# Optimization experiments

Hardware: AMD Instinct MI355X
Metric: run time of the kernel (lower is better)

## Reference

```python
import jax, jax.numpy as jnp
import numpy as np
import math

D_MODEL = 1024
N_HEADS = 16
D_K = 64
CHUNK_LEN = 64


def setup_inputs() -> dict:
    key = jax.random.key(0)
    ks = jax.random.split(key, 12)
    hd = N_HEADS * D_K
    s = 0.02
    return {
        'h': jax.random.normal(ks[0], (4, 2048, D_MODEL), jnp.float32),
        'e': jax.random.normal(ks[1], (4, 32, 2, 128, D_MODEL), jnp.float32),
        'Wq': jax.random.normal(ks[2], (D_MODEL, hd), jnp.float32) * s,
        'bq': jnp.zeros((hd,), jnp.float32),
        'Wk': jax.random.normal(ks[3], (D_MODEL, hd), jnp.float32) * s,
        'bk': jnp.zeros((hd,), jnp.float32),
        'Wv': jax.random.normal(ks[4], (D_MODEL, hd), jnp.float32) * s,
        'bv': jnp.zeros((hd,), jnp.float32),
        'Wo': jax.random.normal(ks[5], (hd, D_MODEL), jnp.float32) * s,
        'bo': jnp.zeros((D_MODEL,), jnp.float32),
        'gamma': jnp.ones((D_MODEL,), jnp.float32),
        'beta': jnp.zeros((D_MODEL,), jnp.float32),
    }


def reference(h, e, Wq, bq, Wk, bk, Wv, bv, Wo, bo, gamma, beta):
    b, chunks, neighbors, nlen, d_model = e.shape
    seq_len = h.shape[1]
    scale = 1.0 / math.sqrt(D_K)
    h_res = h
    # shift so chunk i attends to neighbors retrieved for chunk i
    hh = h[:, CHUNK_LEN - 1:]
    # layer norm
    mu = jnp.mean(hh, axis=-1, keepdims=True)
    var = jnp.mean(jnp.square(hh - mu), axis=-1, keepdims=True)
    hh = (hh - mu) / jnp.sqrt(var + 1e-5) * gamma + beta
    # pad to chunks * CHUNK_LEN
    pad = chunks * CHUNK_LEN - hh.shape[1]
    hh = jnp.pad(hh, ((0, 0), (0, pad), (0, 0)))
    hh = hh.reshape(b, chunks, CHUNK_LEN, d_model)
    q = (hh @ Wq + bq).reshape(b, chunks, CHUNK_LEN, N_HEADS, D_K)
    k = (e @ Wk + bk).reshape(b, chunks, neighbors, nlen, N_HEADS, D_K)
    v = (e @ Wv + bv).reshape(b, chunks, neighbors, nlen, N_HEADS, D_K)
    attn = jnp.einsum('bcihd,bcnjhd->bchinj', q, k) * scale  # [b,c,h,i,n,j]
    a_shape = attn.shape
    attn = jax.nn.softmax(attn.reshape(*a_shape[:-2], -1), axis=-1).reshape(a_shape)
    out = jnp.einsum('bchinj,bcnjhd->bcihd', attn, v)
    out = out.reshape(b, chunks * CHUNK_LEN, N_HEADS * D_K)
    out = out @ Wo + bo
    out = jnp.pad(out, ((0, 0), (CHUNK_LEN - 1, 0), (0, 0)))
    return out[:, :seq_len] + h_res
```

## Files before the change

### kernel.cpp

```cpp
#include <hip/hip_runtime.h>
#include <cstdint>
#include <cstddef>


typedef float f32x4 __attribute__((ext_vector_type(4)));
typedef __bf16 bf16x8 __attribute__((ext_vector_type(8)));

static __device__ __forceinline__ ushort f2bf(float f) {
  union { float f; uint32_t u; } x; x.f = f;
  uint32_t r = x.u + 0x7fffu + ((x.u >> 16) & 1u);
  return (ushort)(r >> 16);
}

static __device__ __forceinline__ bf16x8 ld_frag(const ushort* p) {
  union { uint4 u; bf16x8 v; } x;
  x.u = *(const uint4*)p;
  return x.v;
}

static __device__ __forceinline__ bf16x8 u4_frag(uint4 u) {
  union { uint4 u; bf16x8 v; } x;
  x.u = u;
  return x.v;
}

static __device__ __forceinline__ void gl2lds16(const ushort* g, ushort* l) {
  __builtin_amdgcn_global_load_lds(
      (const __attribute__((address_space(1))) void*)g,
      (__attribute__((address_space(3))) void*)l,
      16, 0, 0);
}

__global__ __launch_bounds__(256) void transpose_cast4(const float* __restrict__ Wq,
                                                       const float* __restrict__ Wk,
                                                       const float* __restrict__ Wv,
                                                       const float* __restrict__ Wo,
                                                       ushort* __restrict__ WqT,
                                                       ushort* __restrict__ WkvT,
                                                       ushort* __restrict__ WoT) {
  const float* W; ushort* WT;
  switch (blockIdx.z) {
    case 0:  W = Wq; WT = WqT; break;
    case 1:  W = Wk; WT = WkvT; break;
    case 2:  W = Wv; WT = WkvT + (size_t)1024 * 1024; break;
    default: W = Wo; WT = WoT; break;
  }
  __shared__ float tile[64][65];
  const int t = threadIdx.x;
  const int n0 = blockIdx.x * 64, k0 = blockIdx.y * 64;
#pragma unroll
  for (int i = 0; i < 4; ++i) {
    int lid = i * 256 + t;
    int r = lid >> 4, c4 = (lid & 15) * 4;
    float4 v = *(const float4*)&W[(size_t)(k0 + r) * 1024 + n0 + c4];
    tile[r][c4 + 0] = v.x; tile[r][c4 + 1] = v.y;
    tile[r][c4 + 2] = v.z; tile[r][c4 + 3] = v.w;
  }
  __syncthreads();
#pragma unroll
  for (int i = 0; i < 4; ++i) {
    int lid = i * 256 + t;
    int n = lid >> 4, k4 = (lid & 15) * 4;
    ushort4 o;
    o.x = f2bf(tile[k4 + 0][n]); o.y = f2bf(tile[k4 + 1][n]);
    o.z = f2bf(tile[k4 + 2][n]); o.w = f2bf(tile[k4 + 3][n]);
    *(ushort4*)&WT[(size_t)(n0 + n) * 1024 + k0 + k4] = o;
  }
}

__global__ __launch_bounds__(256) void cast_bf16(const float* __restrict__ x,
                                                 ushort* __restrict__ y) {
  const size_t i = ((size_t)blockIdx.x * 256 + threadIdx.x) * 8;
  float4 a = *(const float4*)&x[i];
  float4 b = *(const float4*)&x[i + 4];
  ushort o[8];
  o[0] = f2bf(a.x); o[1] = f2bf(a.y); o[2] = f2bf(a.z); o[3] = f2bf(a.w);
  o[4] = f2bf(b.x); o[5] = f2bf(b.y); o[6] = f2bf(b.z); o[7] = f2bf(b.w);
  *(uint4*)&y[i] = *(const uint4*)o;
}

__global__ __launch_bounds__(256) void ln_kernel(const float* __restrict__ h,
                                                 const float* __restrict__ gamma,
                                                 const float* __restrict__ beta,
                                                 ushort* __restrict__ hh) {
  const int bx = blockIdx.x;
  const int b = bx >> 11, s = bx & 2047;
  const int t = threadIdx.x;
  ushort* orow = hh + (size_t)(b * 2048 + s) * 1024;
  if (s >= 1985) {
    ushort4 z; z.x = 0; z.y = 0; z.z = 0; z.w = 0;
    *(ushort4*)&orow[t * 4] = z;
    return;
  }
  const float* xrow = h + (size_t)(b * 2048 + 63 + s) * 1024;
  float4 x = *(const float4*)&xrow[t * 4];
  float s1 = x.x + x.y + x.z + x.w;
  float s2 = x.x * x.x + x.y * x.y + x.z * x.z + x.w * x.w;
#pragma unroll
  for (int off = 32; off > 0; off >>= 1) {
    s1 += __shfl_xor(s1, off);
    s2 += __shfl_xor(s2, off);
  }
  __shared__ float a1[4], a2[4];
  if ((t & 63) == 0) { a1[t >> 6] = s1; a2[t >> 6] = s2; }
  __syncthreads();
  s1 = a1[0] + a1[1] + a1[2] + a1[3];
  s2 = a2[0] + a2[1] + a2[2] + a2[3];
  const float mu = s1 * (1.0f / 1024.0f);
  const float var = s2 * (1.0f / 1024.0f) - mu * mu;
  const float rstd = rsqrtf(var + 1e-5f);
  float4 g = *(const float4*)&gamma[t * 4];
  float4 be = *(const float4*)&beta[t * 4];
  ushort4 o;
  o.x = f2bf((x.x - mu) * rstd * g.x + be.x);
  o.y = f2bf((x.y - mu) * rstd * g.y + be.y);
  o.z = f2bf((x.z - mu) * rstd * g.z + be.z);
  o.w = f2bf((x.w - mu) * rstd * g.w + be.w);
  *(ushort4*)&orow[t * 4] = o;
}

template <int MODE, int NT>
__global__ __launch_bounds__(256) void gemm_bf16(const ushort* __restrict__ A,
                                                 const ushort* __restrict__ Bt,
                                                 const float* __restrict__ bias,
                                                 const float* __restrict__ bias2,
                                                 ushort* __restrict__ Cbf,
                                                 ushort* __restrict__ Vtg,
                                                 float* __restrict__ Cf,
                                                 const float* __restrict__ resid,
                                                 int mtiles, float scale,
                                                 int mrow_off) {
  if constexpr (MODE == 1) {
    if (blockIdx.x >= 512) {
      const int idx4 = (blockIdx.x - 512) * 256 + threadIdx.x;
      const int b = idx4 / 16128;
      const int rem = idx4 - b * 16128;
      const size_t o = (size_t)b * 2048 * 1024 + (size_t)rem * 4;
      *(float4*)&Cf[o] = *(const float4*)&resid[o];
      return;
    }
  }
  __shared__ __align__(16) ushort Alds[2][128 * 32];
  __shared__ __align__(16) ushort Blds[2][128 * 32];
  const int t = threadIdx.x;
  const int lane = t & 63, wave = t >> 6;
  const int quad = lane >> 4, l16 = lane & 15;

  const int L = blockIdx.x;
  const int xcd = L & 7, slot = L >> 3;
  const int nt = slot & (NT - 1);
  const int mt = xcd * (mtiles >> 3) + (slot / NT);
  const int m0 = mt * 128, n0 = nt * 128;

  const int srow = lane >> 2;
  const int scol = (lane & 3) * 8;
  const int c0 = wave * 2;
  const ushort* gA0 = A  + (size_t)(m0 + c0 * 16 + srow) * 1024 + scol;
  const ushort* gA1 = gA0 + 16 * 1024;
  const ushort* gB0 = Bt + (size_t)(n0 + c0 * 16 + srow) * 1024 + scol;
  const ushort* gB1 = gB0 + 16 * 1024;
  ushort* dA0 = &Alds[0][c0 * 512 + lane * 8];
  ushort* dA1 = dA0 + 512;
  ushort* dB0 = &Blds[0][c0 * 512 + lane * 8];
  ushort* dB1 = dB0 + 512;
  const ptrdiff_t SUB = 128 * 32;

  const int wrow = (wave >> 1) * 64, wcol = (wave & 1) * 64;
  const ushort* pA = &Alds[0][(wrow + l16) * 32 + quad * 8];
  const ushort* pB = &Blds[0][(wcol + l16) * 32 + quad * 8];

  f32x4 zero = {0.f, 0.f, 0.f, 0.f};
  f32x4 acc[4][4];
#pragma unroll
  for (int i = 0; i < 4; ++i)
#pragma unroll
    for (int j = 0; j < 4; ++j) acc[i][j] = zero;

  for (int kb = 0; kb < 16; ++kb) {
    const int ko = kb * 64;
    gl2lds16(gA0 + ko, dA0);         gl2lds16(gA1 + ko, dA1);
    gl2lds16(gA0 + ko + 32, dA0 + SUB); gl2lds16(gA1 + ko + 32, dA1 + SUB);
    gl2lds16(gB0 + ko, dB0);         gl2lds16(gB1 + ko, dB1);
    gl2lds16(gB0 + ko + 32, dB0 + SUB); gl2lds16(gB1 + ko + 32, dB1 + SUB);
    __syncthreads();
#pragma unroll
    for (int sub = 0; sub < 2; ++sub) {
      bf16x8 af[4], bfv[4];
#pragma unroll
      for (int i = 0; i < 4; ++i) af[i]  = ld_frag(pA + sub * SUB + i * 512);
#pragma unroll
      for (int j = 0; j < 4; ++j) bfv[j] = ld_frag(pB + sub * SUB + j * 512);
#pragma unroll
      for (int i = 0; i < 4; ++i)
#pragma unroll
        for (int j = 0; j < 4; ++j)
          acc[i][j] = __builtin_amdgcn_mfma_f32_16x16x32_bf16(af[i], bfv[j], acc[i][j], 0, 0, 0);
    }
    __syncthreads();
  }

#pragma unroll
  for (int mi = 0; mi < 4; ++mi)
#pragma unroll
    for (int mj = 0; mj < 4; ++mj) {
      const int cc = n0 + wcol + mj * 16 + l16;
      const int r0 = m0 + wrow + mi * 16 + quad * 4;
      if constexpr (MODE == 0) {
        const float bvb = bias[cc];
#pragma unroll
        for (int rr = 0; rr < 4; ++rr)
          Cbf[(size_t)(r0 + rr) * 1024 + cc] = f2bf((acc[mi][mj][rr] + bvb) * scale);
      } else {
        const float bvb = bias[cc];
#pragma unroll
        for (int rr = 0; rr < 4; ++rr) {
          const int r = r0 + rr;
          const int b = r >> 11, s = r & 2047;
          if (s < 1985) {
            const size_t o = (size_t)(b * 2048 + s + 63) * 1024 + cc;
            Cf[o] = acc[mi][mj][rr] + bvb + resid[o];
          }
        }
      }
    }
}

__global__ __launch_bounds__(512, 2) void gemm_kv256(const ushort* __restrict__ A,
                                                     const ushort* __restrict__ Bt,
                                                     const float* __restrict__ bk_,
                                                     const float* __restrict__ bv_,
                                                     ushort* __restrict__ Kout,
                                                     ushort* __restrict__ Vtg,
                                                     int mrow_off) {
  __shared__ __align__(16) ushort Alds[4 * 8192];
  __shared__ __align__(16) ushort Blds[4 * 8192];

  const int t = threadIdx.x;
  const int lane = t & 63, wave = t >> 6;
  const int wm = wave >> 2, wn = wave & 3;
  const int l16 = lane & 15, quad = lane >> 4;

  const int L = blockIdx.x;
  const int xcd = L & 7, slot = L >> 3;
  const int nt = slot & 7, mt = xcd * 8 + (slot >> 3);
  const int m0 = mt * 256, n0 = nt * 256;

  const int w2 = wave * 2;
  const int srow = lane >> 3;
  const int lanex = (lane & 7) ^ srow;
  const ushort* gA2 = A  + (size_t)(m0 + w2 * 8 + srow) * 1024 + lanex * 8;
  const ushort* gB2 = Bt + (size_t)(n0 + w2 * 8 + srow) * 1024 + lanex * 8;
  ushort* dA2 = Alds + w2 * 512 + lane * 8;
  ushort* dB2 = Blds + w2 * 512 + lane * 8;

  auto stage_a = [&](int ti, int hh) {
    const ushort* g = gA2 + (size_t)hh * 131072 + (size_t)ti * 64;
    ushort* d = dA2 + ((ti & 1) * 2 + hh) * 8192;
    gl2lds16(g, d);
    gl2lds16(g + 8192, d + 512);
  };
  auto stage_b = [&](int ti, int hh) {
    const ushort* g = gB2 + (size_t)hh * 131072 + (size_t)ti * 64;
    ushort* d = dB2 + ((ti & 1) * 2 + hh) * 8192;
    gl2lds16(g, d);
    gl2lds16(g + 8192, d + 512);
  };

  const int b2 = (l16 >> 2) & 1;
  const int qx = (quad ^ (l16 & 3)) << 3;
  const int kof0 = b2 << 5;
  const int kof1 = 32 - kof0;

  f32x4 zero = {0.f, 0.f, 0.f, 0.f};
  f32x4 acc[8][4];
#pragma unroll
  for (int i = 0; i < 8; ++i)
#pragma unroll
    for (int j = 0; j < 4; ++j) acc[i][j] = zero;

  stage_b(0, 0); stage_a(0, 0); stage_b(0, 1); stage_a(0, 1);
  stage_b(1, 0); stage_a(1, 0); stage_b(1, 1);
  asm volatile("s_waitcnt vmcnt(6)" ::: "memory");
  __builtin_amdgcn_s_barrier();

  bf16x8 a[4][2], b01[2][2], b23[2][2];

#pragma unroll 2
  for (int tt = 0; tt < 16; ++tt) {
    const int cur = tt & 1;
    const ushort* pa = Alds + (cur * 2 + wm) * 8192 + l16 * 64 + qx;
    const ushort* pb = Blds + (cur * 2 + (wn >> 1)) * 8192 +
                       ((wn & 1) * 64 + l16) * 64 + qx;

#pragma unroll
    for (int mi = 0; mi < 4; ++mi) {
      a[mi][0] = ld_frag(pa + mi * 1024 + kof0);
      a[mi][1] = ld_frag(pa + mi * 1024 + kof1);
    }
#pragma unroll
    for (int ni = 0; ni < 2; ++ni) {
      b01[ni][0] = ld_frag(pb + ni * 1024 + kof0);
      b01[ni][1] = ld_frag(pb + ni * 1024 + kof1);
    }
    if (tt < 15) stage_a(tt + 1, 1);
    __builtin_amdgcn_s_barrier();
    asm volatile("s_waitcnt lgkmcnt(0)" ::: "memory");
    __builtin_amdgcn_sched_barrier(0);
    __builtin_amdgcn_s_setprio(1);
#pragma unroll
    for (int mi = 0; mi < 4; ++mi)
#pragma unroll
      for (int ni = 0; ni < 2; ++ni) {
        acc[mi][ni] = __builtin_amdgcn_mfma_f32_16x16x32_bf16(a[mi][0], b01[ni][0], acc[mi][ni], 0, 0, 0);
        acc[mi][ni] = __builtin_amdgcn_mfma_f32_16x16x32_bf16(a[mi][1], b01[ni][1], acc[mi][ni], 0, 0, 0);
      }
    __builtin_amdgcn_s_setprio(0);
    __builtin_amdgcn_s_barrier();

#pragma unroll
    for (int ni = 0; ni < 2; ++ni) {
      b23[ni][0] = ld_frag(pb + (ni + 2) * 1024 + kof0);
      b23[ni][1] = ld_frag(pb + (ni + 2) * 1024 + kof1);
    }
    if (tt < 14) stage_b(tt + 2, 0);
    __builtin_amdgcn_s_barrier();
    asm volatile("s_waitcnt lgkmcnt(0)" ::: "memory");
    __builtin_amdgcn_sched_barrier(0);
    __builtin_amdgcn_s_setprio(1);
#pragma unroll
    for (int mi = 0; mi < 4; ++mi)
#pragma unroll
      for (int ni = 0; ni < 2; ++ni) {
        acc[mi][ni + 2] = __builtin_amdgcn_mfma_f32_16x16x32_bf16(a[mi][0], b23[ni][0], acc[mi][ni + 2], 0, 0, 0);
        acc[mi][ni + 2] = __builtin_amdgcn_mfma_f32_16x16x32_bf16(a[mi][1], b23[ni][1], acc[mi][ni + 2], 0, 0, 0);
      }
    __builtin_amdgcn_s_setprio(0);
    __builtin_amdgcn_s_barrier();

#pragma unroll
    for (int mi = 0; mi < 4; ++mi) {
      a[mi][0] = ld_frag(pa + (mi + 4) * 1024 + kof0);
      a[mi][1] = ld_frag(pa + (mi + 4) * 1024 + kof1);
    }
    if (tt < 14) stage_b(tt + 2, 1);
    __builtin_amdgcn_s_barrier();
    asm volatile("s_waitcnt lgkmcnt(0)" ::: "memory");
    __builtin_amdgcn_sched_barrier(0);
    __builtin_amdgcn_s_setprio(1);
#pragma unroll
    for (int mi = 0; mi < 4; ++mi)
#pragma unroll
      for (int ni = 0; ni < 2; ++ni) {
        acc[mi + 4][ni + 2] = __builtin_amdgcn_mfma_f32_16x16x32_bf16(a[mi][0], b23[ni][0], acc[mi + 4][ni + 2], 0, 0, 0);
        acc[mi + 4][ni + 2] = __builtin_amdgcn_mfma_f32_16x16x32_bf16(a[mi][1], b23[ni][1], acc[mi + 4][ni + 2], 0, 0, 0);
      }
    __builtin_amdgcn_s_setprio(0);
    __builtin_amdgcn_s_barrier();

    if (tt < 14) stage_a(tt + 2, 0);
    __builtin_amdgcn_s_barrier();
    __builtin_amdgcn_s_setprio(1);
#pragma unroll
    for (int mi = 0; mi < 4; ++mi)
#pragma unroll
      for (int ni = 0; ni < 2; ++ni) {
        acc[mi + 4][ni] = __builtin_amdgcn_mfma_f32_16x16x32_bf16(a[mi][0], b01[ni][0], acc[mi + 4][ni], 0, 0, 0);
        acc[mi + 4][ni] = __builtin_amdgcn_mfma_f32_16x16x32_bf16(a[mi][1], b01[ni][1], acc[mi + 4][ni], 0, 0, 0);
      }
    __builtin_amdgcn_s_setprio(0);
    if (tt < 15) {
      if (tt == 14) asm volatile("s_waitcnt vmcnt(0)" ::: "memory");
      else          asm volatile("s_waitcnt vmcnt(6)" ::: "memory");
      __builtin_amdgcn_s_barrier();
    }
  }

  const int rbase = m0 + wm * 128 + quad * 4;
  const int cbase = n0 + wn * 64 + l16;
  if (n0 < 1024) {
#pragma unroll
    for (int mi = 0; mi < 8; ++mi)
#pragma unroll
      for (int ni = 0; ni < 4; ++ni) {
        const int cc = cbase + ni * 16;
        const float bb = bk_[cc];
        const int r0 = rbase + mi * 16;
#pragma unroll
        for (int rr = 0; rr < 4; ++rr)
          Kout[(size_t)(r0 + rr) * 1024 + cc] = f2bf(acc[mi][ni][rr] + bb);
      }
  } else {
#pragma unroll
    for (int mi = 0; mi < 8; ++mi)
#pragma unroll
      for (int ni = 0; ni < 4; ++ni) {
        const int cv = cbase - 1024 + ni * 16;
        const int hh_ = cv >> 6, dd = cv & 63;
        const float bb = bv_[cv];
        const int gr0 = rbase + mi * 16 + mrow_off;
        const int bcl = gr0 >> 8, j0 = gr0 & 255;
        ushort4 o;
        o.x = f2bf(acc[mi][ni][0] + bb);
        o.y = f2bf(acc[mi][ni][1] + bb);
        o.z = f2bf(acc[mi][ni][2] + bb);
        o.w = f2bf(acc[mi][ni][3] + bb);
        *(ushort4*)&Vtg[(size_t)(bcl * 16 + hh_) * 16384 + dd * 256 + j0] = o;
      }
  }
}

__global__ __launch_bounds__(256, 3) void attn_kernel(const ushort* __restrict__ Qb,
                                                      const ushort* __restrict__ Kb,
                                                      const ushort* __restrict__ Vtg,
                                                      ushort* __restrict__ Ob) {
  __shared__ __align__(16) ushort Qs[64 * 72];
  __shared__ __align__(16) ushort Ps[64 * 264];
  __shared__ float redm[4][64];
  __shared__ float reds[4][64];

  const int t = threadIdx.x;
  const int bx = blockIdx.x;
  const int hd = bx & 15, c = (bx >> 4) & 31, b = bx >> 9;
  const int lane = t & 63, wave = t >> 6;
  const int quad = lane >> 4, l16 = lane & 15;

  const int qrow0 = b * 2048 + c * 64;
  const int kvrow0 = (b * 32 + c) * 256;
  const int colh = hd * 64;
  const ushort* vsrc = Vtg + ((size_t)((b * 32 + c) * 16 + hd)) * 16384;

  const int jw = wave * 64;
  bf16x8 kf[4][2];
#pragma unroll
  for (int mj = 0; mj < 4; ++mj)
#pragma unroll
    for (int kb = 0; kb < 2; ++kb)
      kf[mj][kb] = ld_frag(&Kb[(size_t)(kvrow0 + jw + mj * 16 + l16) * 1024 +
                               colh + kb * 32 + quad * 8]);

#pragma unroll
  for (int it = 0; it < 2; ++it) {
    int lid = it * 256 + t;
    uint4 v = *(const uint4*)&Qb[(size_t)(qrow0 + (lid >> 3)) * 1024 + colh + (lid & 7) * 8];
    *(uint4*)&Qs[(lid >> 3) * 72 + (lid & 7) * 8] = v;
  }
  __syncthreads();

  f32x4 zero = {0.f, 0.f, 0.f, 0.f};
  f32x4 acc[4][4];
#pragma unroll
  for (int i = 0; i < 4; ++i)
#pragma unroll
    for (int j = 0; j < 4; ++j) acc[i][j] = zero;

  __builtin_amdgcn_s_setprio(1);
#pragma unroll
  for (int kb = 0; kb < 2; ++kb) {
    bf16x8 af[4];
#pragma unroll
    for (int mi = 0; mi < 4; ++mi)
      af[mi] = ld_frag(&Qs[(mi * 16 + l16) * 72 + kb * 32 + quad * 8]);
#pragma unroll
    for (int mi = 0; mi < 4; ++mi)
#pragma unroll
      for (int mj = 0; mj < 4; ++mj)
        acc[mi][mj] = __builtin_amdgcn_mfma_f32_16x16x32_bf16(af[mi], kf[mj][kb], acc[mi][mj], 0, 0, 0);
  }
  __builtin_amdgcn_s_setprio(0);

  const int d0 = wave * 16;
  bf16x8 vf[8];
#pragma unroll
  for (int kb = 0; kb < 8; ++kb)
    vf[kb] = ld_frag(&vsrc[(d0 + l16) * 256 + kb * 32 + quad * 8]);

  float rmax[4][4];
#pragma unroll
  for (int mi = 0; mi < 4; ++mi)
#pragma unroll
    for (int rr = 0; rr < 4; ++rr) {
      float m = fmaxf(fmaxf(acc[mi][0][rr], acc[mi][1][rr]),
                      fmaxf(acc[mi][2][rr], acc[mi][3][rr]));
      m = fmaxf(m, __shfl_xor(m, 1));
      m = fmaxf(m, __shfl_xor(m, 2));
      m = fmaxf(m, __shfl_xor(m, 4));
      m = fmaxf(m, __shfl_xor(m, 8));
      rmax[mi][rr] = m;
    }
  if (l16 == 0) {
#pragma unroll
    for (int mi = 0; mi < 4; ++mi)
#pragma unroll
      for (int rr = 0; rr < 4; ++rr)
        redm[wave][mi * 16 + quad * 4 + rr] = rmax[mi][rr];
  }
  __syncthreads();
  float gmax[4][4];
#pragma unroll
  for (int mi = 0; mi < 4; ++mi)
#pragma unroll
    for (int rr = 0; rr < 4; ++rr) {
      const int row = mi * 16 + quad * 4 + rr;
      gmax[mi][rr] = fmaxf(fmaxf(redm[0][row], redm[1][row]),
                           fmaxf(redm[2][row], redm[3][row]));
    }
  float rsum[4][4];
#pragma unroll
  for (int mi = 0; mi < 4; ++mi)
#pragma unroll
    for (int rr = 0; rr < 4; ++rr) {
      float s = 0.f;
#pragma unroll
      for (int mj = 0; mj < 4; ++mj) {
        float p = exp2f((acc[mi][mj][rr] - gmax[mi][rr]) * 1.4426950408889634f);
        acc[mi][mj][rr] = p;
        s += p;
      }
      s += __shfl_xor(s, 1);
      s += __shfl_xor(s, 2);
      s += __shfl_xor(s, 4);
      s += __shfl_xor(s, 8);
      rsum[mi][rr] = s;
    }
  if (l16 == 0) {
#pragma unroll
    for (int mi = 0; mi < 4; ++mi)
#pragma unroll
      for (int rr = 0; rr < 4; ++rr)
        reds[wave][mi * 16 + quad * 4 + rr] = rsum[mi][rr];
  }
  __syncthreads();
#pragma unroll
  for (int mi = 0; mi < 4; ++mi)
#pragma unroll
    for (int rr = 0; rr < 4; ++rr) {
      const int row = mi * 16 + quad * 4 + rr;
      const float inv = 1.0f / (reds[0][row] + reds[1][row] + reds[2][row] + reds[3][row]);
#pragma unroll
      for (int mj = 0; mj < 4; ++mj)
        Ps[row * 264 + jw + mj * 16 + l16] = f2bf(acc[mi][mj][rr] * inv);
    }
  __syncthreads();

  f32x4 acc2[4];
#pragma unroll
  for (int mi = 0; mi < 4; ++mi) acc2[mi] = zero;
  __builtin_amdgcn_s_setprio(1);
#pragma unroll
  for (int kb = 0; kb < 8; ++kb) {
#pragma unroll
    for (int mi = 0; mi < 4; ++mi) {
      bf16x8 af = ld_frag(&Ps[(mi * 16 + l16) * 264 + kb * 32 + quad * 8]);
      acc2[mi] = __builtin_amdgcn_mfma_f32_16x16x32_bf16(af, vf[kb], acc2[mi], 0, 0, 0);
    }
  }
  __builtin_amdgcn_s_setprio(0);
#pragma unroll
  for (int mi = 0; mi < 4; ++mi)
#pragma unroll
    for (int rr = 0; rr < 4; ++rr) {
      const int i = mi * 16 + quad * 4 + rr;
      Ob[(size_t)(qrow0 + i) * 1024 + colh + d0 + l16] = f2bf(acc2[mi][rr]);
    }
}

extern "C" void kernel_launch(void* const* d_in, const int* in_sizes, int n_in,
                              void* d_out, int out_size, void* d_ws, size_t ws_size,
                              hipStream_t stream) {
  const float* h     = (const float*)d_in[0];
  const float* e     = (const float*)d_in[1];
  const float* Wq    = (const float*)d_in[2];
  const float* bq    = (const float*)d_in[3];
  const float* Wk    = (const float*)d_in[4];
  const float* bk    = (const float*)d_in[5];
  const float* Wv    = (const float*)d_in[6];
  const float* bv    = (const float*)d_in[7];
  const float* Wo    = (const float*)d_in[8];
  const float* bo    = (const float*)d_in[9];
  const float* gamma = (const float*)d_in[10];
  const float* beta  = (const float*)d_in[11];
  float* out = (float*)d_out;

  char* ws = (char*)d_ws;
  ushort* stg  = (ushort*)(ws + ((size_t)0 << 20));
  ushort* WqT  = (ushort*)(ws + ((size_t)32 << 20));
  ushort* WkvT = (ushort*)(ws + ((size_t)34 << 20));
  ushort* WoT  = (ushort*)(ws + ((size_t)38 << 20));
  ushort* Qb   = (ushort*)(ws + ((size_t)40 << 20));
  ushort* Kb   = (ushort*)(ws + ((size_t)56 << 20));
  ushort* VtG  = (ushort*)(ws + ((size_t)120 << 20));

  transpose_cast4<<<dim3(16, 16, 4), 256, 0, stream>>>(Wq, Wk, Wv, Wo, WqT, WkvT, WoT);

  ln_kernel<<<8192, 256, 0, stream>>>(h, gamma, beta, stg);

  gemm_bf16<0, 8><<<512, 256, 0, stream>>>(stg, WqT, bq, nullptr, Qb, nullptr,
                                           nullptr, nullptr, 64, 0.125f, 0);

  for (int half = 0; half < 2; ++half) {
    const size_t roff = (size_t)half * 16384 * 1024;
    cast_bf16<<<8192, 256, 0, stream>>>(e + roff, stg);
    gemm_kv256<<<512, 512, 0, stream>>>(stg, WkvT, bk, bv, Kb + roff,
                                        VtG, half * 16384);
  }

  attn_kernel<<<2048, 256, 0, stream>>>(Qb, Kb, VtG, stg);

  gemm_bf16<1, 8><<<764, 256, 0, stream>>>(stg, WoT, bo, nullptr, nullptr, nullptr,
                                           out, h, 64, 1.0f, 0);
}
```

Baseline: 503.9 us.

## Restructure attention as one wave per head with online softmax

Result: no change. 502.1 us (-0.4%).

```diff
diff --git a/kernel.cpp b/kernel.cpp
--- a/kernel.cpp
+++ b/kernel.cpp
@@ -15,12 +15,6 @@
 static __device__ __forceinline__ bf16x8 ld_frag(const ushort* p) {
   union { uint4 u; bf16x8 v; } x;
   x.u = *(const uint4*)p;
-  return x.v;
-}
-
-static __device__ __forceinline__ bf16x8 u4_frag(uint4 u) {
-  union { uint4 u; bf16x8 v; } x;
-  x.u = u;
   return x.v;
 }
 
@@ -409,159 +403,143 @@
   }
 }
 
-__global__ __launch_bounds__(256, 3) void attn_kernel(const ushort* __restrict__ Qb,
+__global__ __launch_bounds__(256, 2) void attn_kernel(const ushort* __restrict__ Qb,
                                                       const ushort* __restrict__ Kb,
                                                       const ushort* __restrict__ Vtg,
                                                       ushort* __restrict__ Ob) {
-  __shared__ __align__(16) ushort Qs[64 * 72];
-  __shared__ __align__(16) ushort Ps[64 * 264];
-  __shared__ float redm[4][64];
-  __shared__ float reds[4][64];
+  __shared__ __align__(16) ushort Plds[4][4096];
 
   const int t = threadIdx.x;
-  const int bx = blockIdx.x;
-  const int hd = bx & 15, c = (bx >> 4) & 31, b = bx >> 9;
   const int lane = t & 63, wave = t >> 6;
   const int quad = lane >> 4, l16 = lane & 15;
+  const int hw = blockIdx.x * 4 + wave;
+  const int hd = hw & 15, c = (hw >> 4) & 31, b = hw >> 9;
 
   const int qrow0 = b * 2048 + c * 64;
   const int kvrow0 = (b * 32 + c) * 256;
   const int colh = hd * 64;
   const ushort* vsrc = Vtg + ((size_t)((b * 32 + c) * 16 + hd)) * 16384;
-
-  const int jw = wave * 64;
-  bf16x8 kf[4][2];
-#pragma unroll
-  for (int mj = 0; mj < 4; ++mj)
-#pragma unroll
-    for (int kb = 0; kb < 2; ++kb)
-      kf[mj][kb] = ld_frag(&Kb[(size_t)(kvrow0 + jw + mj * 16 + l16) * 1024 +
-                               colh + kb * 32 + quad * 8]);
-
-#pragma unroll
-  for (int it = 0; it < 2; ++it) {
-    int lid = it * 256 + t;
-    uint4 v = *(const uint4*)&Qb[(size_t)(qrow0 + (lid >> 3)) * 1024 + colh + (lid & 7) * 8];
-    *(uint4*)&Qs[(lid >> 3) * 72 + (lid & 7) * 8] = v;
-  }
-  __syncthreads();
+  char* pw = (char*)&Plds[wave][0];
+  const int swz = (l16 & 7) << 4;
+
+  bf16x8 qf[4][2];
+#pragma unroll
+  for (int qq = 0; qq < 4; ++qq)
+#pragma unroll
+    for (int cc = 0; cc < 2; ++cc)
+      qf[qq][cc] = ld_frag(&Qb[(size_t)(qrow0 + qq * 16 + l16) * 1024 +
+                               colh + cc * 32 + quad * 8]);
 
   f32x4 zero = {0.f, 0.f, 0.f, 0.f};
-  f32x4 acc[4][4];
-#pragma unroll
-  for (int i = 0; i < 4; ++i)
-#pragma unroll
-    for (int j = 0; j < 4; ++j) acc[i][j] = zero;
-
-  __builtin_amdgcn_s_setprio(1);
-#pragma unroll
-  for (int kb = 0; kb < 2; ++kb) {
-    bf16x8 af[4];
-#pragma unroll
-    for (int mi = 0; mi < 4; ++mi)
-      af[mi] = ld_frag(&Qs[(mi * 16 + l16) * 72 + kb * 32 + quad * 8]);
-#pragma unroll
-    for (int mi = 0; mi < 4; ++mi)
-#pragma unroll
-      for (int mj = 0; mj < 4; ++mj)
-        acc[mi][mj] = __builtin_amdgcn_mfma_f32_16x16x32_bf16(af[mi], kf[mj][kb], acc[mi][mj], 0, 0, 0);
-  }
-  __builtin_amdgcn_s_setprio(0);
-
-  const int d0 = wave * 16;
-  bf16x8 vf[8];
-#pragma unroll
-  for (int kb = 0; kb < 8; ++kb)
-    vf[kb] = ld_frag(&vsrc[(d0 + l16) * 256 + kb * 32 + quad * 8]);
-
-  float rmax[4][4];
-#pragma unroll
-  for (int mi = 0; mi < 4; ++mi)
-#pragma unroll
-    for (int rr = 0; rr < 4; ++rr) {
-      float m = fmaxf(fmaxf(acc[mi][0][rr], acc[mi][1][rr]),
-                      fmaxf(acc[mi][2][rr], acc[mi][3][rr]));
-      m = fmaxf(m, __shfl_xor(m, 1));
-      m = fmaxf(m, __shfl_xor(m, 2));
-      m = fmaxf(m, __shfl_xor(m, 4));
-      m = fmaxf(m, __shfl_xor(m, 8));
-      rmax[mi][rr] = m;
-    }
-  if (l16 == 0) {
-#pragma unroll
-    for (int mi = 0; mi < 4; ++mi)
-#pragma unroll
-      for (int rr = 0; rr < 4; ++rr)
-        redm[wave][mi * 16 + quad * 4 + rr] = rmax[mi][rr];
-  }
-  __syncthreads();
-  float gmax[4][4];
-#pragma unroll
-  for (int mi = 0; mi < 4; ++mi)
-#pragma unroll
-    for (int rr = 0; rr < 4; ++rr) {
-      const int row = mi * 16 + quad * 4 + rr;
-      gmax[mi][rr] = fmaxf(fmaxf(redm[0][row], redm[1][row]),
-                           fmaxf(redm[2][row], redm[3][row]));
-    }
-  float rsum[4][4];
-#pragma unroll
-  for (int mi = 0; mi < 4; ++mi)
-#pragma unroll
-    for (int rr = 0; rr < 4; ++rr) {
-      float s = 0.f;
-#pragma unroll
-      for (int mj = 0; mj < 4; ++mj) {
-        float p = exp2f((acc[mi][mj][rr] - gmax[mi][rr]) * 1.4426950408889634f);
-        acc[mi][mj][rr] = p;
-        s += p;
-      }
-      s += __shfl_xor(s, 1);
-      s += __shfl_xor(s, 2);
-      s += __shfl_xor(s, 4);
-      s += __shfl_xor(s, 8);
-      rsum[mi][rr] = s;
-    }
-  if (l16 == 0) {
-#pragma unroll
-    for (int mi = 0; mi < 4; ++mi)
-#pragma unroll
-      for (int rr = 0; rr < 4; ++rr)
-        reds[wave][mi * 16 + quad * 4 + rr] = rsum[mi][rr];
-  }
-  __syncthreads();
-#pragma unroll
-  for (int mi = 0; mi < 4; ++mi)
-#pragma unroll
-    for (int rr = 0; rr < 4; ++rr) {
-      const int row = mi * 16 + quad * 4 + rr;
-      const float inv = 1.0f / (reds[0][row] + reds[1][row] + reds[2][row] + reds[3][row]);
-#pragma unroll
-      for (int mj = 0; mj < 4; ++mj)
-        Ps[row * 264 + jw + mj * 16 + l16] = f2bf(acc[mi][mj][rr] * inv);
-    }
-  __syncthreads();
-
-  f32x4 acc2[4];
-#pragma unroll
-  for (int mi = 0; mi < 4; ++mi) acc2[mi] = zero;
-  __builtin_amdgcn_s_setprio(1);
-#pragma unroll
-  for (int kb = 0; kb < 8; ++kb) {
-#pragma unroll
-    for (int mi = 0; mi < 4; ++mi) {
-      bf16x8 af = ld_frag(&Ps[(mi * 16 + l16) * 264 + kb * 32 + quad * 8]);
-      acc2[mi] = __builtin_amdgcn_mfma_f32_16x16x32_bf16(af, vf[kb], acc2[mi], 0, 0, 0);
-    }
-  }
-  __builtin_amdgcn_s_setprio(0);
-#pragma unroll
-  for (int mi = 0; mi < 4; ++mi)
-#pragma unroll
-    for (int rr = 0; rr < 4; ++rr) {
-      const int i = mi * 16 + quad * 4 + rr;
-      Ob[(size_t)(qrow0 + i) * 1024 + colh + d0 + l16] = f2bf(acc2[mi][rr]);
-    }
+  f32x4 Ot[4][4];
+#pragma unroll
+  for (int dd = 0; dd < 4; ++dd)
+#pragma unroll
+    for (int qq = 0; qq < 4; ++qq) Ot[dd][qq] = zero;
+  float m[4], l[4];
+#pragma unroll
+  for (int qq = 0; qq < 4; ++qq) { m[qq] = -1e30f; l[qq] = 0.f; }
+
+  for (int kb = 0; kb < 4; ++kb) {
+    bf16x8 kf[4][2];
+#pragma unroll
+    for (int kk = 0; kk < 4; ++kk)
+#pragma unroll
+      for (int cc = 0; cc < 2; ++cc)
+        kf[kk][cc] = ld_frag(&Kb[(size_t)(kvrow0 + kb * 64 + kk * 16 + l16) * 1024 +
+                                 colh + cc * 32 + quad * 8]);
+
+    f32x4 st[4][4];
+#pragma unroll
+    for (int kk = 0; kk < 4; ++kk)
+#pragma unroll
+      for (int qq = 0; qq < 4; ++qq) st[kk][qq] = zero;
+#pragma unroll
+    for (int cc = 0; cc < 2; ++cc)
+#pragma unroll
+      for (int kk = 0; kk < 4; ++kk)
+#pragma unroll
+        for (int qq = 0; qq < 4; ++qq)
+          st[kk][qq] = __builtin_amdgcn_mfma_f32_16x16x32_bf16(kf[kk][cc], qf[qq][cc], st[kk][qq], 0, 0, 0);
+
+    bf16x8 vf[4][2];
+#pragma unroll
+    for (int dd = 0; dd < 4; ++dd)
+#pragma unroll
+      for (int cc = 0; cc < 2; ++cc)
+        vf[dd][cc] = ld_frag(&vsrc[(dd * 16 + l16) * 256 + kb * 64 + cc * 32 + quad * 8]);
+
+#pragma unroll
+    for (int qq = 0; qq < 4; ++qq) {
+      float bm = st[0][qq][0];
+#pragma unroll
+      for (int kk = 0; kk < 4; ++kk)
+#pragma unroll
+        for (int rr = 0; rr < 4; ++rr) bm = fmaxf(bm, st[kk][qq][rr]);
+      bm = fmaxf(bm, __shfl_xor(bm, 16));
+      bm = fmaxf(bm, __shfl_xor(bm, 32));
+      const float mn = fmaxf(m[qq], bm);
+      const float sc = exp2f(m[qq] - mn);
+      float bs = 0.f;
+#pragma unroll
+      for (int kk = 0; kk < 4; ++kk)
+#pragma unroll
+        for (int rr = 0; rr < 4; ++rr) {
+          float p = exp2f(st[kk][qq][rr] - mn);
+          st[kk][qq][rr] = p;
+          bs += p;
+        }
+      bs += __shfl_xor(bs, 16);
+      bs += __shfl_xor(bs, 32);
+      l[qq] = l[qq] * sc + bs;
+      m[qq] = mn;
+#pragma unroll
+      for (int dd = 0; dd < 4; ++dd) Ot[dd][qq] *= sc;
+      const int rowb = (qq * 16 + l16) * 128;
+#pragma unroll
+      for (int kk = 0; kk < 4; ++kk) {
+        uint32_t w0 = (uint32_t)f2bf(st[kk][qq][0]) | ((uint32_t)f2bf(st[kk][qq][1]) << 16);
+        uint32_t w1 = (uint32_t)f2bf(st[kk][qq][2]) | ((uint32_t)f2bf(st[kk][qq][3]) << 16);
+        const int byte = rowb + ((kk * 32 + quad * 8) ^ swz);
+        *(uint32_t*)(pw + byte) = w0;
+        *(uint32_t*)(pw + byte + 4) = w1;
+      }
+    }
+
+#pragma unroll
+    for (int qq = 0; qq < 4; ++qq)
+#pragma unroll
+      for (int cc = 0; cc < 2; ++cc) {
+        const int byte = (qq * 16 + l16) * 128 + ((cc * 64 + quad * 16) ^ swz);
+        bf16x8 pf = ld_frag((const ushort*)(pw + byte));
+#pragma unroll
+        for (int dd = 0; dd < 4; ++dd)
+          Ot[dd][qq] = __builtin_amdgcn_mfma_f32_16x16x32_bf16(vf[dd][cc], pf, Ot[dd][qq], 0, 0, 0);
+      }
+  }
+
+#pragma unroll
+  for (int qq = 0; qq < 4; ++qq) {
+    const float inv = 1.0f / l[qq];
+    const int rowb = (qq * 16 + l16) * 128;
+#pragma unroll
+    for (int dd = 0; dd < 4; ++dd) {
+      f32x4 v = Ot[dd][qq];
+      uint32_t w0 = (uint32_t)f2bf(v[0] * inv) | ((uint32_t)f2bf(v[1] * inv) << 16);
+      uint32_t w1 = (uint32_t)f2bf(v[2] * inv) | ((uint32_t)f2bf(v[3] * inv) << 16);
+      const int byte = rowb + ((dd * 32 + quad * 8) ^ swz);
+      *(uint32_t*)(pw + byte) = w0;
+      *(uint32_t*)(pw + byte + 4) = w1;
+    }
+  }
+#pragma unroll
+  for (int p = 0; p < 8; ++p) {
+    const int r = p * 8 + (lane >> 3);
+    const int ch = lane & 7;
+    const int byte = r * 128 + ((ch * 16) ^ ((r & 7) << 4));
+    uint4 o = *(const uint4*)(pw + byte);
+    *(uint4*)&Ob[(size_t)(qrow0 + r) * 1024 + colh + ch * 8] = o;
+  }
 }
 
 extern "C" void kernel_launch(void* const* d_in, const int* in_sizes, int n_in,
@@ -595,7 +573,8 @@
   ln_kernel<<<8192, 256, 0, stream>>>(h, gamma, beta, stg);
 
   gemm_bf16<0, 8><<<512, 256, 0, stream>>>(stg, WqT, bq, nullptr, Qb, nullptr,
-                                           nullptr, nullptr, 64, 0.125f, 0);
+                                           nullptr, nullptr, 64,
+                                           0.125f * 1.4426950408889634f, 0);
 
   for (int half = 0; half < 2; ++half) {
     const size_t roff = (size_t)half * 16384 * 1024;
@@ -604,7 +583,7 @@
                                         VtG, half * 16384);
   }
 
-  attn_kernel<<<2048, 256, 0, stream>>>(Qb, Kb, VtG, stg);
+  attn_kernel<<<512, 256, 0, stream>>>(Qb, Kb, VtG, stg);
 
   gemm_bf16<1, 8><<<764, 256, 0, stream>>>(stg, WoT, bo, nullptr, nullptr, nullptr,
                                            out, h, 64, 1.0f, 0);
```
